# Kernel tuning notes

Hardware: AMD Instinct MI355X
Metric: run time of the kernel (lower is better)

The kernel has to match this reference:

```python
import jax, jax.numpy as jnp
import numpy as np

EPS = 1e-5

def _batchnorm(x, gamma, beta):
    # BatchNorm1d in training mode: stats over the point (N) dimension, biased var
    mean = x.mean(axis=0)
    var = ((x - mean) ** 2).mean(axis=0)
    return (x - mean) * jax.lax.rsqrt(var + EPS) * gamma + beta

def setup_inputs() -> dict:
    key = jax.random.key(0)
    ks = jax.random.split(key, 6)
    N, C_in, K, B = 262144, 3, 64, 16
    return {
        "feats": jax.random.normal(ks[0], (N, C_in), dtype=jnp.float32),
        "batch_idx": jax.random.randint(ks[1], (N,), 0, B, dtype=jnp.int32),
        "W1": jax.random.normal(ks[2], (128, C_in), dtype=jnp.float32) * 0.1,
        "gamma1": jnp.ones((128,), jnp.float32),
        "beta1": jnp.zeros((128,), jnp.float32),
        "W2": jax.random.normal(ks[3], (64, 256), dtype=jnp.float32) * 0.05,
        "gamma2": jnp.ones((64,), jnp.float32),
        "beta2": jnp.zeros((64,), jnp.float32),
        "W3": jax.random.normal(ks[4], (K, 64), dtype=jnp.float32) * 0.1,
        "b3": jnp.zeros((K,), jnp.float32),
        "num_batches": B,
    }

def reference(feats, batch_idx, W1, gamma1, beta1, W2, gamma2, beta2, W3, b3, num_batches):
    # conv1 (1x1 conv == linear, no bias) + bn1
    x = _batchnorm(feats @ W1.T, gamma1, beta1)          # [N,128]
    # per-batch global max pooling, broadcast back to points
    seg_max = jax.ops.segment_max(x, batch_idx, num_segments=num_batches)  # [B,128]
    x = jnp.concatenate([x, seg_max[batch_idx]], axis=1)  # [N,256]
    # conv2 + bn2 + relu
    x = jax.nn.relu(_batchnorm(x @ W2.T, gamma2, beta2))  # [N,64]
    # conv3 (with bias)
    return x @ W3.T + b3                                   # [N,k]
```

## Files before the change

kernel.cpp:

```cpp
#include <hip/hip_runtime.h>
#include <hip/hip_bf16.h>

#define EPS 1e-5f
#define NPTS 262144
#define NB 16
#define ACBLK 1024

typedef __attribute__((ext_vector_type(8))) short bf16x8;
typedef __attribute__((ext_vector_type(4))) float f32x4;

#define WS_E    0
#define WS_T    192
#define WS_W3   1216
#define WS_MAXG 3264
#define WS_PMOM 5312
#define WS_SCRM 6480
#define WS_PART 81232
#define WS_SMAX 114000

__device__ inline float decodeu(unsigned u){
  unsigned bits = (u & 0x80000000u) ? (u ^ 0x80000000u) : ~u;
  return __uint_as_float(bits);
}
__device__ inline unsigned f2bf(float f){
  unsigned u = __float_as_uint(f);
  return (u + 0x7FFFu + ((u>>16)&1u)) >> 16;
}
__device__ inline unsigned pack2bf(float lo, float hi){
  return (f2bf(hi)<<16) | (f2bf(lo) & 0xFFFFu);
}
__device__ inline unsigned ordu(float v){
  unsigned bits = __float_as_uint(v);
  return bits ^ (unsigned)(((int)bits>>31) | (int)0x80000000);
}

__global__ __launch_bounds__(256) void kAC(const float* __restrict__ feats,
                                           const int* __restrict__ bidx,
                                           const float* __restrict__ W1,
                                           const float* __restrict__ g1,
                                           float* __restrict__ wsf, int mode) {
  __shared__ unsigned lmax[NB*128];
  __shared__ __align__(16) float4 sfeat[256];
  __shared__ float hist[NB*4];
  __shared__ float red[4*9];
  int tid = threadIdx.x;
  for (int i=tid;i<NB*128;i+=256) lmax[i]=0u;
  if (tid < NB*4) hist[tid]=0.f;
  __syncthreads();
  int p = blockIdx.x*256 + tid;
  float f0=feats[3*p], f1=feats[3*p+1], f2=feats[3*p+2];
  int b = bidx[p];
  sfeat[tid] = make_float4(f0,f1,f2,__int_as_float(b));
  atomicAdd(&hist[b*4+0],f0);
  atomicAdd(&hist[b*4+1],f1);
  atomicAdd(&hist[b*4+2],f2);
  atomicAdd(&hist[b*4+3],1.0f);
  int lane = tid&63, wv = tid>>6;
  { float acc[9]={f0,f1,f2,f0*f0,f0*f1,f0*f2,f1*f1,f1*f2,f2*f2};
    #pragma unroll
    for (int k=0;k<9;k++){
      float v=acc[k];
      v+=__shfl_down(v,32); v+=__shfl_down(v,16); v+=__shfl_down(v,8);
      v+=__shfl_down(v,4);  v+=__shfl_down(v,2);  v+=__shfl_down(v,1);
      if (lane==0) red[wv*9+k]=v;
    }
  }
  __syncthreads();
  int c0 = lane, c1 = lane+64;
  float sg0 = (g1[c0]>=0.f)?1.f:-1.f;
  float sg1 = (g1[c1]>=0.f)?1.f:-1.f;
  float w00=W1[3*c0]*sg0, w01=W1[3*c0+1]*sg0, w02=W1[3*c0+2]*sg0;
  float w10=W1[3*c1]*sg1, w11=W1[3*c1+1]*sg1, w12=W1[3*c1+2]*sg1;
  const float4* sp = &sfeat[wv*64];
  float m0[16], m1[16];
  #pragma unroll
  for (int q=0;q<16;q++){ m0[q] = -__builtin_inff(); m1[q] = -__builtin_inff(); }
  #pragma unroll 8
  for (int k=0;k<64;k++){
    float4 f = sp[k];
    float v0 = fmaf(f.z,w02,fmaf(f.y,w01,f.x*w00));
    float v1 = fmaf(f.z,w12,fmaf(f.y,w11,f.x*w10));
    int sbb = __builtin_amdgcn_readfirstlane(__float_as_int(f.w));
    switch (sbb){
      case 0:  m0[0]=fmaxf(m0[0],v0);  m1[0]=fmaxf(m1[0],v1);  break;
      case 1:  m0[1]=fmaxf(m0[1],v0);  m1[1]=fmaxf(m1[1],v1);  break;
      case 2:  m0[2]=fmaxf(m0[2],v0);  m1[2]=fmaxf(m1[2],v1);  break;
      case 3:  m0[3]=fmaxf(m0[3],v0);  m1[3]=fmaxf(m1[3],v1);  break;
      case 4:  m0[4]=fmaxf(m0[4],v0);  m1[4]=fmaxf(m1[4],v1);  break;
      case 5:  m0[5]=fmaxf(m0[5],v0);  m1[5]=fmaxf(m1[5],v1);  break;
      case 6:  m0[6]=fmaxf(m0[6],v0);  m1[6]=fmaxf(m1[6],v1);  break;
      case 7:  m0[7]=fmaxf(m0[7],v0);  m1[7]=fmaxf(m1[7],v1);  break;
      case 8:  m0[8]=fmaxf(m0[8],v0);  m1[8]=fmaxf(m1[8],v1);  break;
      case 9:  m0[9]=fmaxf(m0[9],v0);  m1[9]=fmaxf(m1[9],v1);  break;
      case 10: m0[10]=fmaxf(m0[10],v0); m1[10]=fmaxf(m1[10],v1); break;
      case 11: m0[11]=fmaxf(m0[11],v0); m1[11]=fmaxf(m1[11],v1); break;
      case 12: m0[12]=fmaxf(m0[12],v0); m1[12]=fmaxf(m1[12],v1); break;
      case 13: m0[13]=fmaxf(m0[13],v0); m1[13]=fmaxf(m1[13],v1); break;
      case 14: m0[14]=fmaxf(m0[14],v0); m1[14]=fmaxf(m1[14],v1); break;
      default: m0[15]=fmaxf(m0[15],v0); m1[15]=fmaxf(m1[15],v1); break;
    }
  }
  #pragma unroll
  for (int q=0;q<16;q++){
    if (m0[q] > -__builtin_inff()) atomicMax(&lmax[q*128+c0], ordu(m0[q]));
    if (m1[q] > -__builtin_inff()) atomicMax(&lmax[q*128+c1], ordu(m1[q]));
  }
  __syncthreads();
  float* scrM = wsf + WS_SCRM + blockIdx.x*73;
  if (tid<9) scrM[tid]=red[tid]+red[9+tid]+red[18+tid]+red[27+tid];
  if (tid>=64 && tid<128) scrM[9+tid-64]=hist[tid-64];
  if (mode){
    unsigned* spo = (unsigned*)wsf + WS_SMAX + (size_t)blockIdx.x*2048;
    for (int i=tid;i<2048;i+=256) spo[i]=lmax[i];
  } else {
    unsigned* mg = (unsigned*)wsf + WS_MAXG;
    for (int i=tid;i<2048;i+=256){ unsigned v=lmax[i]; if(v) atomicMax(&mg[i],v); }
  }
}

__global__ __launch_bounds__(256) void kM(float* __restrict__ wsf){
  int g = blockIdx.x >> 3, ec = blockIdx.x & 7;
  int e = ec*256 + threadIdx.x;
  const unsigned* smax = (const unsigned*)wsf + WS_SMAX;
  unsigned m = 0;
  #pragma unroll 4
  for (int k=g*64;k<g*64+64;k++){ unsigned t=smax[(size_t)k*2048+e]; m = t>m?t:m; }
  ((unsigned*)wsf)[WS_PART + g*2048 + e] = m;
  if (ec==0 && threadIdx.x<73){
    float s=0; const float* sm0 = wsf + WS_SCRM;
    #pragma unroll 4
    for (int k=g*64;k<g*64+64;k++) s += sm0[k*73+threadIdx.x];
    wsf[WS_PMOM + g*73 + threadIdx.x] = s;
  }
}

__global__ __launch_bounds__(1024) void kB(float* __restrict__ wsf,
    const float* __restrict__ W1, const float* __restrict__ g1, const float* __restrict__ b1,
    const float* __restrict__ W2, const float* __restrict__ g2, const float* __restrict__ b2,
    const float* __restrict__ W3, int mode) {
  __shared__ __align__(16) float4 w2q[64*66];
  __shared__ __align__(16) float4 smbnq[NB*32];
  __shared__ __align__(16) float4 srhsq[4*32];
  __shared__ float s_w1[384];
  __shared__ float s_sc[128], s_sh[128], sE[3*64], sg[64], sT[NB*64];
  __shared__ float smom[80], s_s2[64], s_t2[64];
  int tid = threadIdx.x;
  float4 rw[4];
  #pragma unroll
  for (int t=0;t<4;t++) rw[t] = ((const float4*)W2)[tid + t*1024];
  float4 rw3 = ((const float4*)W3)[tid];
  if (tid<384) s_w1[tid]=W1[tid];
  #pragma unroll
  for (int t=0;t<4;t++){
    int q = tid + t*1024;
    w2q[(q&63)*66 + (q>>6)] = rw[t];
  }
  { unsigned* w3u = (unsigned*)wsf + WS_W3;
    w3u[2*tid]   = pack2bf(rw3.x, rw3.y);
    w3u[2*tid+1] = pack2bf(rw3.z, rw3.w);
  }
  if (mode){
    if (tid<73){ float s=0;
      #pragma unroll
      for (int g=0;g<16;g++) s += wsf[WS_PMOM+g*73+tid];
      smom[tid]=s; }
  } else {
    if (tid<73){ float s=0; const float* sm0=wsf+WS_SCRM;
      for (int k=0;k<ACBLK;k++) s += sm0[k*73+tid];
      smom[tid]=s; }
  }
  __syncthreads();
  const float invN = 1.0f/NPTS;
  if (tid < 128){
    int c=tid; float w0=s_w1[3*c],w1=s_w1[3*c+1],w2=s_w1[3*c+2];
    float mean = (w0*smom[0]+w1*smom[1]+w2*smom[2])*invN;
    float ex2 = (w0*w0*smom[3]+w1*w1*smom[6]+w2*w2*smom[8]
               + 2.f*(w0*w1*smom[4]+w0*w2*smom[5]+w1*w2*smom[7]))*invN;
    float var = ex2 - mean*mean;
    float sc = g1[c]*rsqrtf(var+EPS);
    s_sc[c]=sc; s_sh[c]=b1[c]-mean*sc;
  }
  __syncthreads();
  { const unsigned* part=(const unsigned*)wsf+WS_PART;
    const unsigned* mg=(const unsigned*)wsf+WS_MAXG;
    float* smbnf = (float*)smbnq;
    #pragma unroll
    for (int i=tid;i<NB*128;i+=1024){
      unsigned u;
      if (mode){ u=0;
        #pragma unroll
        for (int g=0;g<16;g++){ unsigned t=part[g*2048+i]; u = t>u?t:u; }
      } else u = mg[i];
      float M = decodeu(u);
      int ch=i&127;
      smbnf[i] = fabsf(s_sc[ch])*M + s_sh[ch];
    } }
  if (tid < 512){
    int which = tid>>7, j = tid&127;
    ((float*)srhsq)[tid] = (which<3) ? s_sc[j]*s_w1[3*j+which] : s_sh[j];
  }
  __syncthreads();
  { int c = tid&63, b = tid>>6;
    const float4* rq = &smbnq[b*32];
    float s=0;
    #pragma unroll 8
    for (int jj=0;jj<32;jj++){
      float4 a = w2q[(32+jj)*66 + c];
      float4 r = rq[jj];
      s = fmaf(a.x,r.x,fmaf(a.y,r.y,fmaf(a.z,r.z,fmaf(a.w,r.w,s))));
    }
    sT[b*64+c] = s;
    if (tid < 256){
      int which = tid>>6;
      float s2=0;
      #pragma unroll 8
      for (int jj=0;jj<32;jj++){
        float4 a = w2q[jj*66 + c];
        float4 r = srhsq[which*32+jj];
        s2 = fmaf(a.x,r.x,fmaf(a.y,r.y,fmaf(a.z,r.z,fmaf(a.w,r.w,s2))));
      }
      if (which<3) sE[which*64+c]=s2; else sg[c]=s2;
    }
  }
  __syncthreads();
  if (tid < 64){
    int c=tid;
    float e0=sE[c],e1=sE[64+c],e2=sE[128+c],gc=sg[c];
    float sumY = e0*smom[0]+e1*smom[1]+e2*smom[2];
    float sumYY = e0*e0*smom[3]+e1*e1*smom[6]+e2*e2*smom[8]
               + 2.f*(e0*e1*smom[4]+e0*e2*smom[5]+e1*e2*smom[7]);
    #pragma unroll
    for (int b=0;b<NB;b++){
      float nb = smom[9+b*4+3];
      float hb = gc + sT[b*64+c];
      float eS1b = e0*smom[9+b*4]+e1*smom[9+b*4+1]+e2*smom[9+b*4+2];
      sumY += nb*hb;
      sumYY += 2.f*hb*eS1b + nb*hb*hb;
    }
    float mean2 = sumY*invN;
    float var2 = sumYY*invN - mean2*mean2;
    float s2 = g2[c]*rsqrtf(var2+EPS);
    float t2 = b2[c]-mean2*s2;
    s_s2[c]=s2; s_t2[c]=t2;
    wsf[WS_E + c] = e0*s2; wsf[WS_E+64+c]=e1*s2; wsf[WS_E+128+c]=e2*s2;
  }
  __syncthreads();
  { int c=tid&63;
    if (tid < NB*64) wsf[WS_T + tid] = (sg[c]+sT[tid])*s_s2[c] + s_t2[c];
  }
}

__global__ __launch_bounds__(256, 4) void kF(const float* __restrict__ feats,
                                             const int* __restrict__ bidx,
                                             const float* __restrict__ wsf,
                                             const float* __restrict__ b3,
                                             float* __restrict__ out) {
  __shared__ __align__(16) unsigned char SB[36992];
  unsigned* zbuf = (unsigned*)SB;
  float* Tl = (float*)(SB + 32768);
  float* fbuf = (float*)SB;
  int tid = threadIdx.x;
  for (int i=tid;i<NB*64;i+=256) Tl[(i>>6)*66 + (i&63)] = wsf[WS_T + i];
  int lane = tid & 63, wv = tid >> 6;
  int col = lane & 15, kgrp = lane >> 4;
  const ushort* w3b = (const ushort*)((const unsigned*)wsf + WS_W3);
  bf16x8 bfr[4][2];
  #pragma unroll
  for (int n=0;n<4;n++)
    #pragma unroll
    for (int kk=0;kk<2;kk++)
      bfr[n][kk] = *(const bf16x8*)(w3b + (n*16+col)*64 + kk*32 + kgrp*8);
  float bias[4];
  #pragma unroll
  for (int n=0;n<4;n++) bias[n] = b3[n*16+col];
  __syncthreads();
  const float* Eg = wsf + WS_E;
  int p0 = (blockIdx.x*4 + wv)*64;
  int p = p0 + lane;
  float f0 = feats[3*p], f1 = feats[3*p+1], f2 = feats[3*p+2];
  int b = bidx[p];
  const float* tb = &Tl[b*66];
  unsigned rowbase = (unsigned)(wv*64+lane)*32;
  unsigned sw = (lane&7)<<2;
  #pragma unroll
  for (int j=0;j<8;j++){
    unsigned w[4];
    #pragma unroll
    for (int q=0;q<4;q++){
      int c = j*8 + q*2;
      float2 tp = *(const float2*)(tb + c);
      float y0 = fmaf(Eg[c],  f0, fmaf(Eg[64+c],  f1, fmaf(Eg[128+c],  f2, tp.x)));
      float y1 = fmaf(Eg[c+1],f0, fmaf(Eg[64+c+1],f1, fmaf(Eg[128+c+1],f2, tp.y)));
      w[q] = pack2bf(fmaxf(y0,0.f), fmaxf(y1,0.f));
    }
    uint4 ch; ch.x=w[0]; ch.y=w[1]; ch.z=w[2]; ch.w=w[3];
    *(uint4*)&zbuf[rowbase + (((unsigned)(j*4)) ^ sw)] = ch;
  }
  __syncthreads();
  bf16x8 af[4][2];
  #pragma unroll
  for (int m=0;m<4;m++){
    int row = m*16 + col;
    unsigned rb = (unsigned)(wv*64+row)*32;
    unsigned sw2 = (unsigned)(row&7)<<2;
    #pragma unroll
    for (int kk=0;kk<2;kk++){
      unsigned off = ((unsigned)(kk*16 + kgrp*4)) ^ sw2;
      af[m][kk] = *(const bf16x8*)&zbuf[rb + off];
    }
  }
  __syncthreads();
  #pragma unroll
  for (int half=0; half<2; half++){
    f32x4 acc[2][4];
    #pragma unroll
    for (int mi=0;mi<2;mi++)
      #pragma unroll
      for (int n=0;n<4;n++)
        acc[mi][n] = (f32x4){0.f,0.f,0.f,0.f};
    #pragma unroll
    for (int kk=0;kk<2;kk++)
      #pragma unroll
      for (int mi=0;mi<2;mi++)
        #pragma unroll
        for (int n=0;n<4;n++)
          acc[mi][n] = __builtin_amdgcn_mfma_f32_16x16x32_bf16(af[half*2+mi][kk], bfr[n][kk], acc[mi][n], 0,0,0);
    #pragma unroll
    for (int mi=0;mi<2;mi++){
      #pragma unroll
      for (int n=0;n<4;n++){
        #pragma unroll
        for (int r=0;r<4;r++)
          fbuf[wv*2176 + (mi*16 + kgrp*4 + r)*68 + n*16 + col] = acc[mi][n][r] + bias[n];
      }
    }
    __syncthreads();
    #pragma unroll
    for (int it=0; it<8; it++){
      int idx = it*256 + tid;
      int gr = idx >> 4;
      int c4 = (idx & 15) * 4;
      float4 v = *(const float4*)&fbuf[(gr>>5)*2176 + (gr&31)*68 + c4];
      int orow = blockIdx.x*256 + (gr>>5)*64 + half*32 + (gr&31);
      *(float4*)&out[(size_t)orow*64 + c4] = v;
    }
    __syncthreads();
  }
}

extern "C" void kernel_launch(void* const* d_in, const int* in_sizes, int n_in,
                              void* d_out, int out_size, void* d_ws, size_t ws_size,
                              hipStream_t stream) {
  const float* feats = (const float*)d_in[0];
  const int*   bidx  = (const int*)d_in[1];
  const float* W1 = (const float*)d_in[2];
  const float* g1 = (const float*)d_in[3];
  const float* b1 = (const float*)d_in[4];
  const float* W2 = (const float*)d_in[5];
  const float* g2 = (const float*)d_in[6];
  const float* b2 = (const float*)d_in[7];
  const float* W3 = (const float*)d_in[8];
  const float* b3 = (const float*)d_in[9];
  float* wsf = (float*)d_ws;
  float* out = (float*)d_out;
  size_t need = (size_t)(WS_SMAX + (size_t)ACBLK*2048)*4;
  int mode = (ws_size >= need) ? 1 : 0;
  if (!mode) (void)hipMemsetAsync((char*)d_ws + (size_t)WS_MAXG*4, 0, 2048*4, stream);
  kAC<<<ACBLK, 256, 0, stream>>>(feats, bidx, W1, g1, wsf, mode);
  if (mode) kM<<<128, 256, 0, stream>>>(wsf);
  kB<<<1, 1024, 0, stream>>>(wsf, W1,g1,b1, W2,g2,b2, W3, mode);
  kF<<<1024, 256, 0, stream>>>(feats, bidx, wsf, b3, out);
}
```

Before: 60.30 us.

## Replace per-block max dump and reduce kernel with filtered global atomicMax

Drops the mode that wrote each block's 2048-entry segment-max table to the workspace and reduced it in a separate kernel. Each block now folds its local maxima into one global table with atomicMax, skipping the atomic when a plain read shows the stored value is already larger. The moment-sum reduction moves into the single-block kB kernel, which splits the work across 8 thread groups per moment. This removes one kernel launch and about 8 MB of workspace traffic, at the cost of atomic contention on 2048 addresses and a memset.

```diff
diff --git a/kernel.cpp b/kernel.cpp
--- a/kernel.cpp
+++ b/kernel.cpp
@@ -13,10 +13,7 @@
 #define WS_T    192
 #define WS_W3   1216
 #define WS_MAXG 3264
-#define WS_PMOM 5312
 #define WS_SCRM 6480
-#define WS_PART 81232
-#define WS_SMAX 114000
 
 __device__ inline float decodeu(unsigned u){
   unsigned bits = (u & 0x80000000u) ? (u ^ 0x80000000u) : ~u;
@@ -38,7 +35,7 @@
                                            const int* __restrict__ bidx,
                                            const float* __restrict__ W1,
                                            const float* __restrict__ g1,
-                                           float* __restrict__ wsf, int mode) {
+                                           float* __restrict__ wsf) {
   __shared__ unsigned lmax[NB*128];
   __shared__ __align__(16) float4 sfeat[256];
   __shared__ float hist[NB*4];
@@ -109,47 +106,36 @@
   float* scrM = wsf + WS_SCRM + blockIdx.x*73;
   if (tid<9) scrM[tid]=red[tid]+red[9+tid]+red[18+tid]+red[27+tid];
   if (tid>=64 && tid<128) scrM[9+tid-64]=hist[tid-64];
-  if (mode){
-    unsigned* spo = (unsigned*)wsf + WS_SMAX + (size_t)blockIdx.x*2048;
-    for (int i=tid;i<2048;i+=256) spo[i]=lmax[i];
-  } else {
-    unsigned* mg = (unsigned*)wsf + WS_MAXG;
-    for (int i=tid;i<2048;i+=256){ unsigned v=lmax[i]; if(v) atomicMax(&mg[i],v); }
-  }
-}
-
-__global__ __launch_bounds__(256) void kM(float* __restrict__ wsf){
-  int g = blockIdx.x >> 3, ec = blockIdx.x & 7;
-  int e = ec*256 + threadIdx.x;
-  const unsigned* smax = (const unsigned*)wsf + WS_SMAX;
-  unsigned m = 0;
-  #pragma unroll 4
-  for (int k=g*64;k<g*64+64;k++){ unsigned t=smax[(size_t)k*2048+e]; m = t>m?t:m; }
-  ((unsigned*)wsf)[WS_PART + g*2048 + e] = m;
-  if (ec==0 && threadIdx.x<73){
-    float s=0; const float* sm0 = wsf + WS_SCRM;
-    #pragma unroll 4
-    for (int k=g*64;k<g*64+64;k++) s += sm0[k*73+threadIdx.x];
-    wsf[WS_PMOM + g*73 + threadIdx.x] = s;
-  }
+  { unsigned* mg = (unsigned*)wsf + WS_MAXG;
+    for (int i=tid;i<2048;i+=256){
+      unsigned v = lmax[i];
+      if (v > mg[i]) atomicMax(&mg[i], v);
+    } }
 }
 
 __global__ __launch_bounds__(1024) void kB(float* __restrict__ wsf,
     const float* __restrict__ W1, const float* __restrict__ g1, const float* __restrict__ b1,
     const float* __restrict__ W2, const float* __restrict__ g2, const float* __restrict__ b2,
-    const float* __restrict__ W3, int mode) {
+    const float* __restrict__ W3) {
   __shared__ __align__(16) float4 w2q[64*66];
   __shared__ __align__(16) float4 smbnq[NB*32];
   __shared__ __align__(16) float4 srhsq[4*32];
   __shared__ float s_w1[384];
   __shared__ float s_sc[128], s_sh[128], sE[3*64], sg[64], sT[NB*64];
   __shared__ float smom[80], s_s2[64], s_t2[64];
+  __shared__ float pmred[73*8];
   int tid = threadIdx.x;
   float4 rw[4];
   #pragma unroll
   for (int t=0;t<4;t++) rw[t] = ((const float4*)W2)[tid + t*1024];
   float4 rw3 = ((const float4*)W3)[tid];
   if (tid<384) s_w1[tid]=W1[tid];
+  { int m = tid>>3, g = tid&7;
+    if (m<73){
+      float s=0; const float* sm0=wsf+WS_SCRM;
+      for (int k=g*128;k<(g+1)*128;k++) s += sm0[k*73+m];
+      pmred[m*8+g]=s;
+    } }
   #pragma unroll
   for (int t=0;t<4;t++){
     int q = tid + t*1024;
@@ -159,15 +145,12 @@
     w3u[2*tid]   = pack2bf(rw3.x, rw3.y);
     w3u[2*tid+1] = pack2bf(rw3.z, rw3.w);
   }
-  if (mode){
-    if (tid<73){ float s=0;
-      #pragma unroll
-      for (int g=0;g<16;g++) s += wsf[WS_PMOM+g*73+tid];
-      smom[tid]=s; }
-  } else {
-    if (tid<73){ float s=0; const float* sm0=wsf+WS_SCRM;
-      for (int k=0;k<ACBLK;k++) s += sm0[k*73+tid];
-      smom[tid]=s; }
+  __syncthreads();
+  if (tid<73){
+    float s=0;
+    #pragma unroll
+    for (int g=0;g<8;g++) s += pmred[tid*8+g];
+    smom[tid]=s;
   }
   __syncthreads();
   const float invN = 1.0f/NPTS;
@@ -181,17 +164,11 @@
     s_sc[c]=sc; s_sh[c]=b1[c]-mean*sc;
   }
   __syncthreads();
-  { const unsigned* part=(const unsigned*)wsf+WS_PART;
-    const unsigned* mg=(const unsigned*)wsf+WS_MAXG;
+  { const unsigned* mg=(const unsigned*)wsf+WS_MAXG;
     float* smbnf = (float*)smbnq;
     #pragma unroll
     for (int i=tid;i<NB*128;i+=1024){
-      unsigned u;
-      if (mode){ u=0;
-        #pragma unroll
-        for (int g=0;g<16;g++){ unsigned t=part[g*2048+i]; u = t>u?t:u; }
-      } else u = mg[i];
-      float M = decodeu(u);
+      float M = decodeu(mg[i]);
       int ch=i&127;
       smbnf[i] = fabsf(s_sc[ch])*M + s_sh[ch];
     } }
@@ -363,11 +340,8 @@
   const float* b3 = (const float*)d_in[9];
   float* wsf = (float*)d_ws;
   float* out = (float*)d_out;
-  size_t need = (size_t)(WS_SMAX + (size_t)ACBLK*2048)*4;
-  int mode = (ws_size >= need) ? 1 : 0;
-  if (!mode) (void)hipMemsetAsync((char*)d_ws + (size_t)WS_MAXG*4, 0, 2048*4, stream);
-  kAC<<<ACBLK, 256, 0, stream>>>(feats, bidx, W1, g1, wsf, mode);
-  if (mode) kM<<<128, 256, 0, stream>>>(wsf);
-  kB<<<1, 1024, 0, stream>>>(wsf, W1,g1,b1, W2,g2,b2, W3, mode);
-  kF<<<1024, 256, 0, stream>>>(feats, bidx, wsf, b3, out);
-}
+  (void)hipMemsetAsync((char*)d_ws + (size_t)WS_MAXG*4, 0, 2048*4, stream);
+  kAC<<<ACBLK, 256, 0, stream>>>(feats, bidx, W1, g1, wsf);
+  kB<<<1, 1024, 0, stream>>>(wsf, W1,g1,b1, W2,g2,b2, W3);
+  kF<<<ACBLK, 256, 0, stream>>>(feats, bidx, wsf, b3, out);
+}
```

Measured after the change: 96.85 us. +60.6%, slower.
